# Kernel optimization log

Hardware: AMD Instinct MI355X
Metric: run time of the kernel (lower is better)

The kernel has to match this reference:

```python
import jax, jax.numpy as jnp
import numpy as np

B, T, F = 16, 16384, 32
C = 64          # residual_channels == skip_channels
L = 10          # num_layers
K = 3           # kernel_size
OUT = 1
DILATIONS = [2 ** (i % 10) for i in range(L)]


def causal_conv1d(x, w, b, dilation):
    # x: [B,C_in,T], w: [C_out,C_in,K] -> [B,C_out,T], left-padded (causal)
    pad = (w.shape[-1] - 1) * dilation
    y = jax.lax.conv_general_dilated(
        x, w, window_strides=(1,), padding=[(pad, 0)],
        rhs_dilation=(dilation,), dimension_numbers=('NCT', 'OIT', 'NCT'))
    return y + b[None, :, None]


def conv1x1(x, w, b):
    # x: [B,C_in,T], w: [C_out,C_in] -> [B,C_out,T]
    return jnp.einsum('oi,bit->bot', w, x) + b[None, :, None]


def setup_inputs() -> dict:
    key = jax.random.key(0)
    ks = jax.random.split(key, 16)
    s = 0.1
    inp = {
        'x': jax.random.normal(ks[0], (B, T, F), jnp.float32),
        'w_in': jax.random.normal(ks[1], (C, F, 1), jnp.float32) * s,
        'b_in': jnp.zeros((C,), jnp.float32),
        'fw': jax.random.normal(ks[2], (L, C, C, K), jnp.float32) * s,
        'fb': jnp.zeros((L, C), jnp.float32),
        'gw': jax.random.normal(ks[3], (L, C, C, K), jnp.float32) * s,
        'gb': jnp.zeros((L, C), jnp.float32),
        'rw': jax.random.normal(ks[4], (L, C, C), jnp.float32) * s,
        'rb': jnp.zeros((L, C), jnp.float32),
        'sw': jax.random.normal(ks[5], (L, C, C), jnp.float32) * s,
        'sb': jnp.zeros((L, C), jnp.float32),
        'ow1': jax.random.normal(ks[6], (C, C), jnp.float32) * s,
        'ob1': jnp.zeros((C,), jnp.float32),
        'ow2': jax.random.normal(ks[7], (OUT, C), jnp.float32) * s,
        'ob2': jnp.zeros((OUT,), jnp.float32),
    }
    return inp


def reference(x, w_in, b_in, fw, fb, gw, gb, rw, rb, sw, sb, ow1, ob1, ow2, ob2):
    h = jnp.transpose(x, (0, 2, 1))                 # [B,F,T]
    h = causal_conv1d(h, w_in, b_in, 1)             # [B,C,T] (1x1 causal input conv)
    skip_sum = jnp.zeros_like(h[:, :C, :]) * 0.0
    skip_sum = jnp.zeros((h.shape[0], C, h.shape[2]), h.dtype)
    for i, d in enumerate(DILATIONS):
        filt = jnp.tanh(causal_conv1d(h, fw[i], fb[i], d))
        gate = jax.nn.sigmoid(causal_conv1d(h, gw[i], gb[i], d))
        act = filt * gate
        residual = conv1x1(act, rw[i], rb[i])
        skip = conv1x1(act, sw[i], sb[i])
        h = (h + residual) * 0.7071
        skip_sum = skip_sum + skip
    out = jax.nn.relu(skip_sum)
    out = jax.nn.relu(conv1x1(out, ow1, ob1))
    out = conv1x1(out, ow2, ob2)                    # [B,OUT,T]
    return jnp.transpose(out, (0, 2, 1))            # [B,T,OUT]
```

## Files before the change

kernel.cpp:

```cpp
#include <hip/hip_runtime.h>
#include <math.h>

#define Bn 16
#define Tn 16384
#define Fn 32
#define Cn 64
#define Ln 10
#define ST 76

typedef _Float16 v8h  __attribute__((ext_vector_type(8)));
typedef _Float16 v4h  __attribute__((ext_vector_type(4)));
typedef float    v16f __attribute__((ext_vector_type(16)));
typedef float    v4f  __attribute__((ext_vector_type(4)));

__global__ __launch_bounds__(256) void k_prep(const float* __restrict__ fw,
                                              const float* __restrict__ gw,
                                              const float* __restrict__ rw,
                                              const float* __restrict__ sw,
                                              _Float16* __restrict__ wfgP,
                                              _Float16* __restrict__ rsP)
{
    int gid = blockIdx.x * 256 + threadIdx.x;
    if (gid < Ln * 24576) {
        int l      = gid / 24576;
        int rem    = gid % 24576;
        int chunk  = rem >> 9;
        int within = rem & 511;
        int lane   = within >> 3, j = within & 7;
        int ch32 = chunk & 1;
        int fg   = (chunk >> 1) & 1;
        int kc   = (chunk >> 2) & 3;
        int tap  = chunk >> 4;
        int co = ch32 * 32 + (lane & 31);
        int ci = kc * 16 + (lane >> 5) * 8 + j;
        const float* wsrc = fg ? gw : fw;
        wfgP[gid] = (_Float16)wsrc[((l * 64 + co) * 64 + ci) * 3 + tap];
    }
    int gid2 = gid - Ln * 24576;
    if (gid2 >= 0 && gid2 < Ln * 8192) {
        int l      = gid2 / 8192;
        int rem    = gid2 % 8192;
        int chunk  = rem >> 9;
        int within = rem & 511;
        int lane   = within >> 3, j = within & 7;
        int ch32 = chunk & 1;
        int rsi  = (chunk >> 1) & 1;
        int kc   = chunk >> 2;
        int co = ch32 * 32 + (lane & 31);
        int ci = kc * 16 + (lane >> 5) * 8 + j;
        const float* wsrc = rsi ? sw : rw;
        rsP[gid2] = (_Float16)wsrc[(l * 64 + co) * 64 + ci];
    }
}

__device__ __forceinline__ int xcd_swizzle(int bx, int nblk)
{
    return (bx & 7) * (nblk >> 3) + (bx >> 3);
}

__global__ __launch_bounds__(256) void k_input(const float* __restrict__ x,
                                               const float* __restrict__ w_in,
                                               const float* __restrict__ b_in,
                                               _Float16* __restrict__ h)
{
    __shared__ _Float16 HT[256 * 64];
    const int tid = threadIdx.x;
    const int blk = xcd_swizzle(blockIdx.x, Tn / 256);
    const int t0  = blk * 256;
    const int t   = t0 + tid;
    const int bb  = blockIdx.y;
    const float* xp = x + ((size_t)bb * Tn + t) * Fn;
    float xv[32];
    #pragma unroll
    for (int i = 0; i < 8; ++i) {
        v4f v = *(const v4f*)&xp[i * 4];
        xv[i*4+0] = v[0]; xv[i*4+1] = v[1]; xv[i*4+2] = v[2]; xv[i*4+3] = v[3];
    }
    #pragma unroll
    for (int c8 = 0; c8 < 8; ++c8) {
        v8h o;
        #pragma unroll
        for (int j = 0; j < 8; ++j) {
            int c = c8 * 8 + j;
            float a = b_in[c];
            #pragma unroll
            for (int f = 0; f < 32; ++f) a = fmaf(w_in[c * 32 + f], xv[f], a);
            o[j] = (_Float16)a;
        }
        const int p = (c8 + tid) & 7;
        *(v8h*)&HT[tid * 64 + p * 8] = o;
    }
    __syncthreads();
    _Float16* hp = h + ((size_t)bb * Tn + t0) * 64;
    #pragma unroll
    for (int it = 0; it < 8; ++it) {
        const int g  = it * 256 + tid;
        const int tl = g >> 3, c8 = g & 7;
        const int p  = (c8 + tl) & 7;
        *(v8h*)&hp[g * 8] = *(const v8h*)&HT[tl * 64 + p * 8];
    }
}

__global__ __launch_bounds__(256, 4) void k_layer(
    const _Float16* __restrict__ hin, _Float16* __restrict__ hout,
    _Float16* __restrict__ skip,
    const _Float16* __restrict__ wfg,
    const _Float16* __restrict__ rs,
    const float* __restrict__ fb, const float* __restrict__ gb,
    const float* __restrict__ rb, const float* __restrict__ sb,
    const int dil, const float skip_scale)
{
    __shared__ _Float16 P0[64 * ST];
    __shared__ _Float16 P1[64 * ST];

    const int tid  = threadIdx.x;
    const int lane = tid & 63;
    const int wv   = tid >> 6;
    const int ch32 = wv & 1;
    const int ch   = ch32 * 32;
    const int tw   = (wv >> 1) * 32;
    const int hl   = lane >> 5;
    const int ln31 = lane & 31;
    const int bb   = blockIdx.y;
    const int t0   = xcd_swizzle(blockIdx.x, Tn / 64) * 64;
    const size_t hbase = (size_t)bb * Tn * 64;

    v8h zero8;
    #pragma unroll
    for (int j = 0; j < 8; ++j) zero8[j] = (_Float16)0.f;

    const int s_tl = tid >> 3;
    const int s_c  = (tid & 7) * 8;

#define STAGE(DST, OFF) do {                                                  \
    _Pragma("unroll")                                                         \
    for (int it = 0; it < 2; ++it) {                                          \
        int tl = s_tl + it * 32;                                              \
        int tg = t0 + tl - (OFF);                                             \
        v8h v = zero8;                                                        \
        if (tg >= 0) v = *(const v8h*)&hin[hbase + (size_t)tg * 64 + s_c];    \
        *(v8h*)&(DST)[tl * ST + s_c] = v;                                     \
    } } while (0)

#define WOFF(TAP, KC, FG) (((((TAP) * 4 + (KC)) * 2 + (FG)) * 2 + ch32) * 512 + lane * 8)
#define RSOFF(KC, RSI)    ((((KC) * 2 + (RSI)) * 2 + ch32) * 512 + lane * 8)

#define MFMA_TAP(SRC, TAP) do {                                               \
    _Pragma("unroll")                                                         \
    for (int kc = 0; kc < 4; ++kc) {                                          \
        const int kof = kc * 16 + hl * 8;                                     \
        v8h aF = *(const v8h*)&wfg[WOFF(TAP, kc, 0)];                         \
        v8h aG = *(const v8h*)&wfg[WOFF(TAP, kc, 1)];                         \
        v8h b0 = *(const v8h*)&(SRC)[(tw + ln31) * ST + kof];                 \
        accF = __builtin_amdgcn_mfma_f32_32x32x16_f16(aF, b0, accF, 0, 0, 0); \
        accG = __builtin_amdgcn_mfma_f32_32x32x16_f16(aG, b0, accG, 0, 0, 0); \
    } } while (0)

    v16f accF, accG;
    #pragma unroll
    for (int q = 0; q < 4; ++q) {
        v4f fv = *(const v4f*)&fb[ch + 8 * q + 4 * hl];
        v4f gv = *(const v4f*)&gb[ch + 8 * q + 4 * hl];
        #pragma unroll
        for (int r = 0; r < 4; ++r) {
            accF[q * 4 + r] = fv[r];
            accG[q * 4 + r] = gv[r];
        }
    }

    STAGE(P0, 2 * dil);
    __syncthreads();
    STAGE(P1, dil);
    MFMA_TAP(P0, 0);
    __syncthreads();
    STAGE(P0, 0);
    MFMA_TAP(P1, 1);
    __syncthreads();
    MFMA_TAP(P0, 2);

    #pragma unroll
    for (int q = 0; q < 4; ++q) {
        v4h av;
        #pragma unroll
        for (int r = 0; r < 4; ++r) {
            float f = accF[q * 4 + r];
            float g = accG[q * 4 + r];
            float A = __expf(2.f * f);
            float B = __expf(-g);
            float tA = A + 1.f;
            float den = fmaf(tA, B, tA);
            av[r] = (_Float16)((A - 1.f) * __builtin_amdgcn_rcpf(den));
        }
        *(v4h*)&P1[(tw + ln31) * ST + ch + 8 * q + 4 * hl] = av;
    }
    __syncthreads();

    v16f accR, accS;
    #pragma unroll
    for (int q = 0; q < 4; ++q) {
        v4f rv = *(const v4f*)&rb[ch + 8 * q + 4 * hl];
        v4f sv = *(const v4f*)&sb[ch + 8 * q + 4 * hl];
        #pragma unroll
        for (int r = 0; r < 4; ++r) {
            accR[q * 4 + r] = rv[r];
            accS[q * 4 + r] = sv[r];
        }
    }

    #pragma unroll
    for (int kc = 0; kc < 4; ++kc) {
        const int kof = kc * 16 + hl * 8;
        v8h aR = *(const v8h*)&rs[RSOFF(kc, 0)];
        v8h aS = *(const v8h*)&rs[RSOFF(kc, 1)];
        v8h b0 = *(const v8h*)&P1[(tw + ln31) * ST + kof];
        accR = __builtin_amdgcn_mfma_f32_32x32x16_f16(aR, b0, accR, 0, 0, 0);
        accS = __builtin_amdgcn_mfma_f32_32x32x16_f16(aS, b0, accS, 0, 0, 0);
    }

    #pragma unroll
    for (int q = 0; q < 4; ++q) {
        _Float16* cell = &P0[(tw + ln31) * ST + ch + 8 * q + 4 * hl];
        v4h hv = *(const v4h*)cell;
        v4h hn;
        #pragma unroll
        for (int r = 0; r < 4; ++r)
            hn[r] = (_Float16)(((float)hv[r] + accR[q * 4 + r]) * 0.7071f);
        *(v4h*)cell = hn;
    }
    __syncthreads();

    #pragma unroll
    for (int q = 0; q < 4; ++q) {
        v4h sn;
        #pragma unroll
        for (int r = 0; r < 4; ++r)
            sn[r] = (_Float16)accS[q * 4 + r];
        *(v4h*)&P1[(tw + ln31) * ST + ch + 8 * q + 4 * hl] = sn;
    }
    #pragma unroll
    for (int it = 0; it < 2; ++it) {
        int tl = s_tl + it * 32;
        *(v8h*)&hout[hbase + (size_t)(t0 + tl) * 64 + s_c] = *(const v8h*)&P0[tl * ST + s_c];
    }
    __syncthreads();

    #pragma unroll
    for (int it = 0; it < 2; ++it) {
        int tl = s_tl + it * 32;
        const size_t base = hbase + (size_t)(t0 + tl) * 64 + s_c;
        v8h sk = *(const v8h*)&skip[base];
        v8h pv = *(const v8h*)&P1[tl * ST + s_c];
        v8h sn;
        #pragma unroll
        for (int r = 0; r < 8; ++r)
            sn[r] = (_Float16)((float)sk[r] * skip_scale + (float)pv[r]);
        *(v8h*)&skip[base] = sn;
    }
#undef STAGE
#undef MFMA_TAP
#undef WOFF
#undef RSOFF
}

__global__ __launch_bounds__(256) void k_out(const _Float16* __restrict__ skip,
                                             const float* __restrict__ ow1,
                                             const float* __restrict__ ob1,
                                             const float* __restrict__ ow2,
                                             const float* __restrict__ ob2,
                                             float* __restrict__ out)
{
    const int blk = xcd_swizzle(blockIdx.x, Tn / 256);
    const int t  = blk * 256 + threadIdx.x;
    const int bb = blockIdx.y;
    const _Float16* sp = skip + ((size_t)bb * Tn + t) * 64;
    float y[64];
    #pragma unroll
    for (int i = 0; i < 8; ++i) {
        v8h v = *(const v8h*)&sp[i * 8];
        #pragma unroll
        for (int j = 0; j < 8; ++j) y[i * 8 + j] = fmaxf((float)v[j], 0.f);
    }
    float o = ob2[0];
    for (int co = 0; co < 64; ++co) {
        float a0 = ob1[co], a1 = 0.f;
        #pragma unroll
        for (int ci = 0; ci < 64; ci += 2) {
            a0 = fmaf(ow1[co * 64 + ci],     y[ci],     a0);
            a1 = fmaf(ow1[co * 64 + ci + 1], y[ci + 1], a1);
        }
        o = fmaf(ow2[co], fmaxf(a0 + a1, 0.f), o);
    }
    out[(size_t)bb * Tn + t] = o;
}

extern "C" void kernel_launch(void* const* d_in, const int* in_sizes, int n_in,
                              void* d_out, int out_size, void* d_ws, size_t ws_size,
                              hipStream_t stream)
{
    const float* x    = (const float*)d_in[0];
    const float* w_in = (const float*)d_in[1];
    const float* b_in = (const float*)d_in[2];
    const float* fw   = (const float*)d_in[3];
    const float* fb   = (const float*)d_in[4];
    const float* gw   = (const float*)d_in[5];
    const float* gb   = (const float*)d_in[6];
    const float* rw   = (const float*)d_in[7];
    const float* rb   = (const float*)d_in[8];
    const float* sw   = (const float*)d_in[9];
    const float* sb   = (const float*)d_in[10];
    const float* ow1  = (const float*)d_in[11];
    const float* ob1  = (const float*)d_in[12];
    const float* ow2  = (const float*)d_in[13];
    const float* ob2  = (const float*)d_in[14];
    float* out = (float*)d_out;

    const size_t n = (size_t)Bn * Tn * 64;
    _Float16* hA    = (_Float16*)d_ws;
    _Float16* hB    = hA + n;
    _Float16* skip  = hB + n;
    _Float16* wfg16 = skip + n;
    _Float16* rs16  = wfg16 + (size_t)Ln * 24576;

    dim3 blk(256);
    k_prep<<<dim3((Ln * 24576 + Ln * 8192 + 255) / 256), blk, 0, stream>>>(
        fw, gw, rw, sw, wfg16, rs16);
    k_input<<<dim3(Tn / 256, Bn), blk, 0, stream>>>(x, w_in, b_in, hA);

    const _Float16* cur = hA;
    _Float16* nxt = hB;
    for (int l = 0; l < Ln; ++l) {
        const int d = 1 << l;
        k_layer<<<dim3(Tn / 64, Bn), blk, 0, stream>>>(
            cur, nxt, skip,
            wfg16 + (size_t)l * 24576, rs16 + (size_t)l * 8192,
            fb + l * Cn, gb + l * Cn, rb + l * Cn, sb + l * Cn,
            d, (l == 0) ? 0.f : 1.f);
        const _Float16* tmp = nxt; nxt = (_Float16*)cur; cur = tmp;
    }

    k_out<<<dim3(Tn / 256, Bn), blk, 0, stream>>>(skip, ow1, ob1, ow2, ob2, out);
}
```

Before: 549.6 us.

## Add unified-tile layer kernel for small dilations loading one contiguous halo window

Adds a specialized layer kernel for dilations up to 32 that stages a single contiguous 128-row window (64 halo rows plus 64 output rows) into one shared buffer. All three conv taps then read from that buffer, replacing the original kernel's two separate tiles. The buffer is reused for the activations, the updated residual and the skip values. This is meant to cut redundant global loads and shared memory footprint for the first six layers, at the cost of extra barriers and a second code path.

After: 534.7 us. 2.7% less time.

```diff
diff --git a/kernel.cpp b/kernel.cpp
--- a/kernel.cpp
+++ b/kernel.cpp
@@ -99,6 +99,158 @@
         const int p  = (c8 + tl) & 7;
         *(v8h*)&hp[g * 8] = *(const v8h*)&HT[tl * 64 + p * 8];
     }
+}
+
+__global__ __launch_bounds__(256, 4) void k_layer_u(
+    const _Float16* __restrict__ hin, _Float16* __restrict__ hout,
+    _Float16* __restrict__ skip,
+    const _Float16* __restrict__ wfg,
+    const _Float16* __restrict__ rs,
+    const float* __restrict__ fb, const float* __restrict__ gb,
+    const float* __restrict__ rb, const float* __restrict__ sb,
+    const int dil, const float skip_scale)
+{
+    __shared__ _Float16 UB[128 * ST];
+
+    const int tid  = threadIdx.x;
+    const int lane = tid & 63;
+    const int wv   = tid >> 6;
+    const int ch32 = wv & 1;
+    const int ch   = ch32 * 32;
+    const int tw   = (wv >> 1) * 32;
+    const int hl   = lane >> 5;
+    const int ln31 = lane & 31;
+    const int bb   = blockIdx.y;
+    const int t0   = xcd_swizzle(blockIdx.x, Tn / 64) * 64;
+    const size_t hbase = (size_t)bb * Tn * 64;
+
+    v8h zero8;
+    #pragma unroll
+    for (int j = 0; j < 8; ++j) zero8[j] = (_Float16)0.f;
+
+    const int s_tl = tid >> 3;
+    const int s_c  = (tid & 7) * 8;
+
+#define WOFF(TAP, KC, FG) (((((TAP) * 4 + (KC)) * 2 + (FG)) * 2 + ch32) * 512 + lane * 8)
+#define RSOFF(KC, RSI)    ((((KC) * 2 + (RSI)) * 2 + ch32) * 512 + lane * 8)
+
+    #pragma unroll
+    for (int it = 0; it < 4; ++it) {
+        int row = s_tl + it * 32;
+        int tg  = t0 - 64 + row;
+        v8h v = zero8;
+        if (tg >= 0) v = *(const v8h*)&hin[hbase + (size_t)tg * 64 + s_c];
+        *(v8h*)&UB[row * ST + s_c] = v;
+    }
+
+    v16f accF, accG;
+    #pragma unroll
+    for (int q = 0; q < 4; ++q) {
+        v4f fv = *(const v4f*)&fb[ch + 8 * q + 4 * hl];
+        v4f gv = *(const v4f*)&gb[ch + 8 * q + 4 * hl];
+        #pragma unroll
+        for (int r = 0; r < 4; ++r) {
+            accF[q * 4 + r] = fv[r];
+            accG[q * 4 + r] = gv[r];
+        }
+    }
+    __syncthreads();
+
+    #pragma unroll
+    for (int tap = 0; tap < 3; ++tap) {
+        const int rbase = 64 + tw - (2 - tap) * dil;
+        #pragma unroll
+        for (int kc = 0; kc < 4; ++kc) {
+            const int kof = kc * 16 + hl * 8;
+            v8h aF = *(const v8h*)&wfg[WOFF(tap, kc, 0)];
+            v8h aG = *(const v8h*)&wfg[WOFF(tap, kc, 1)];
+            v8h b0 = *(const v8h*)&UB[(rbase + ln31) * ST + kof];
+            accF = __builtin_amdgcn_mfma_f32_32x32x16_f16(aF, b0, accF, 0, 0, 0);
+            accG = __builtin_amdgcn_mfma_f32_32x32x16_f16(aG, b0, accG, 0, 0, 0);
+        }
+    }
+    __syncthreads();
+
+    #pragma unroll
+    for (int q = 0; q < 4; ++q) {
+        v4h av;
+        #pragma unroll
+        for (int r = 0; r < 4; ++r) {
+            float f = accF[q * 4 + r];
+            float g = accG[q * 4 + r];
+            float A = __expf(2.f * f);
+            float B = __expf(-g);
+            float tA = A + 1.f;
+            float den = fmaf(tA, B, tA);
+            av[r] = (_Float16)((A - 1.f) * __builtin_amdgcn_rcpf(den));
+        }
+        *(v4h*)&UB[(tw + ln31) * ST + ch + 8 * q + 4 * hl] = av;
+    }
+    __syncthreads();
+
+    v16f accR, accS;
+    #pragma unroll
+    for (int q = 0; q < 4; ++q) {
+        v4f rv = *(const v4f*)&rb[ch + 8 * q + 4 * hl];
+        v4f sv = *(const v4f*)&sb[ch + 8 * q + 4 * hl];
+        #pragma unroll
+        for (int r = 0; r < 4; ++r) {
+            accR[q * 4 + r] = rv[r];
+            accS[q * 4 + r] = sv[r];
+        }
+    }
+    #pragma unroll
+    for (int kc = 0; kc < 4; ++kc) {
+        const int kof = kc * 16 + hl * 8;
+        v8h aR = *(const v8h*)&rs[RSOFF(kc, 0)];
+        v8h aS = *(const v8h*)&rs[RSOFF(kc, 1)];
+        v8h b0 = *(const v8h*)&UB[(tw + ln31) * ST + kof];
+        accR = __builtin_amdgcn_mfma_f32_32x32x16_f16(aR, b0, accR, 0, 0, 0);
+        accS = __builtin_amdgcn_mfma_f32_32x32x16_f16(aS, b0, accS, 0, 0, 0);
+    }
+
+    #pragma unroll
+    for (int q = 0; q < 4; ++q) {
+        _Float16* cell = &UB[(64 + tw + ln31) * ST + ch + 8 * q + 4 * hl];
+        v4h hv = *(const v4h*)cell;
+        v4h hn;
+        #pragma unroll
+        for (int r = 0; r < 4; ++r)
+            hn[r] = (_Float16)(((float)hv[r] + accR[q * 4 + r]) * 0.7071f);
+        *(v4h*)cell = hn;
+    }
+    __syncthreads();
+
+    #pragma unroll
+    for (int q = 0; q < 4; ++q) {
+        v4h sn;
+        #pragma unroll
+        for (int r = 0; r < 4; ++r)
+            sn[r] = (_Float16)accS[q * 4 + r];
+        *(v4h*)&UB[(tw + ln31) * ST + ch + 8 * q + 4 * hl] = sn;
+    }
+    __syncthreads();
+
+    #pragma unroll
+    for (int it = 0; it < 2; ++it) {
+        int tl = s_tl + it * 32;
+        *(v8h*)&hout[hbase + (size_t)(t0 + tl) * 64 + s_c] =
+            *(const v8h*)&UB[(64 + tl) * ST + s_c];
+    }
+    #pragma unroll
+    for (int it = 0; it < 2; ++it) {
+        int tl = s_tl + it * 32;
+        const size_t base = hbase + (size_t)(t0 + tl) * 64 + s_c;
+        v8h sk = *(const v8h*)&skip[base];
+        v8h pv = *(const v8h*)&UB[tl * ST + s_c];
+        v8h sn;
+        #pragma unroll
+        for (int r = 0; r < 8; ++r)
+            sn[r] = (_Float16)((float)sk[r] * skip_scale + (float)pv[r]);
+        *(v8h*)&skip[base] = sn;
+    }
+#undef WOFF
+#undef RSOFF
 }
 
 __global__ __launch_bounds__(256, 4) void k_layer(
@@ -330,11 +482,19 @@
     _Float16* nxt = hB;
     for (int l = 0; l < Ln; ++l) {
         const int d = 1 << l;
-        k_layer<<<dim3(Tn / 64, Bn), blk, 0, stream>>>(
-            cur, nxt, skip,
-            wfg16 + (size_t)l * 24576, rs16 + (size_t)l * 8192,
-            fb + l * Cn, gb + l * Cn, rb + l * Cn, sb + l * Cn,
-            d, (l == 0) ? 0.f : 1.f);
+        if (d <= 32) {
+            k_layer_u<<<dim3(Tn / 64, Bn), blk, 0, stream>>>(
+                cur, nxt, skip,
+                wfg16 + (size_t)l * 24576, rs16 + (size_t)l * 8192,
+                fb + l * Cn, gb + l * Cn, rb + l * Cn, sb + l * Cn,
+                d, (l == 0) ? 0.f : 1.f);
+        } else {
+            k_layer<<<dim3(Tn / 64, Bn), blk, 0, stream>>>(
+                cur, nxt, skip,
+                wfg16 + (size_t)l * 24576, rs16 + (size_t)l * 8192,
+                fb + l * Cn, gb + l * Cn, rb + l * Cn, sb + l * Cn,
+                d, 1.f);
+        }
         const _Float16* tmp = nxt; nxt = (_Float16*)cur; cur = tmp;
     }
 
```

## Process two 64-step time tiles per block and skip final layer's h write

Applied to the files above, without the earlier changes.

Each layer block now handles 128 time steps as two 64-step sub-tiles, so every weight fragment loaded from global memory feeds four MFMAs instead of two. The last layer no longer computes or writes the residual h output, since nothing reads it. In exchange, LDS use doubles to four 64x76 half buffers and accumulator register pressure doubles. Both changes can lower occupancy, and the grid has half as many blocks.

New measurement: 635.3 us. +15.6%, slower.

```diff
diff --git a/kernel.cpp b/kernel.cpp
--- a/kernel.cpp
+++ b/kernel.cpp
@@ -101,17 +101,18 @@
     }
 }
 
-__global__ __launch_bounds__(256, 4) void k_layer(
+__global__ __launch_bounds__(256, 4) void k_layer2(
     const _Float16* __restrict__ hin, _Float16* __restrict__ hout,
     _Float16* __restrict__ skip,
-    const _Float16* __restrict__ wfg,
-    const _Float16* __restrict__ rs,
+    const _Float16* __restrict__ wfg, const _Float16* __restrict__ rs,
     const float* __restrict__ fb, const float* __restrict__ gb,
     const float* __restrict__ rb, const float* __restrict__ sb,
-    const int dil, const float skip_scale)
+    const int dil, const float skip_scale, const int write_h)
 {
     __shared__ _Float16 P0[64 * ST];
     __shared__ _Float16 P1[64 * ST];
+    __shared__ _Float16 Q0[64 * ST];
+    __shared__ _Float16 Q1[64 * ST];
 
     const int tid  = threadIdx.x;
     const int lane = tid & 63;
@@ -122,7 +123,8 @@
     const int hl   = lane >> 5;
     const int ln31 = lane & 31;
     const int bb   = blockIdx.y;
-    const int t0   = xcd_swizzle(blockIdx.x, Tn / 64) * 64;
+    const int tA   = xcd_swizzle(blockIdx.x, Tn / 128) * 128;
+    const int tB   = tA + 64;
     const size_t hbase = (size_t)bb * Tn * 64;
 
     v8h zero8;
@@ -132,132 +134,167 @@
     const int s_tl = tid >> 3;
     const int s_c  = (tid & 7) * 8;
 
-#define STAGE(DST, OFF) do {                                                  \
+#define STAGE2(DA, DB, OFF) do {                                              \
     _Pragma("unroll")                                                         \
     for (int it = 0; it < 2; ++it) {                                          \
         int tl = s_tl + it * 32;                                              \
-        int tg = t0 + tl - (OFF);                                             \
-        v8h v = zero8;                                                        \
-        if (tg >= 0) v = *(const v8h*)&hin[hbase + (size_t)tg * 64 + s_c];    \
-        *(v8h*)&(DST)[tl * ST + s_c] = v;                                     \
+        int tgA = tA + tl - (OFF);                                            \
+        v8h vA = zero8;                                                       \
+        if (tgA >= 0) vA = *(const v8h*)&hin[hbase + (size_t)tgA * 64 + s_c]; \
+        *(v8h*)&(DA)[tl * ST + s_c] = vA;                                     \
+        int tgB = tB + tl - (OFF);                                            \
+        v8h vB = zero8;                                                       \
+        if (tgB >= 0) vB = *(const v8h*)&hin[hbase + (size_t)tgB * 64 + s_c]; \
+        *(v8h*)&(DB)[tl * ST + s_c] = vB;                                     \
     } } while (0)
 
 #define WOFF(TAP, KC, FG) (((((TAP) * 4 + (KC)) * 2 + (FG)) * 2 + ch32) * 512 + lane * 8)
 #define RSOFF(KC, RSI)    ((((KC) * 2 + (RSI)) * 2 + ch32) * 512 + lane * 8)
 
-#define MFMA_TAP(SRC, TAP) do {                                               \
+#define MFMA_TAP2(SA, SB, TAP) do {                                           \
     _Pragma("unroll")                                                         \
     for (int kc = 0; kc < 4; ++kc) {                                          \
         const int kof = kc * 16 + hl * 8;                                     \
         v8h aF = *(const v8h*)&wfg[WOFF(TAP, kc, 0)];                         \
         v8h aG = *(const v8h*)&wfg[WOFF(TAP, kc, 1)];                         \
-        v8h b0 = *(const v8h*)&(SRC)[(tw + ln31) * ST + kof];                 \
-        accF = __builtin_amdgcn_mfma_f32_32x32x16_f16(aF, b0, accF, 0, 0, 0); \
-        accG = __builtin_amdgcn_mfma_f32_32x32x16_f16(aG, b0, accG, 0, 0, 0); \
+        v8h bA = *(const v8h*)&(SA)[(tw + ln31) * ST + kof];                  \
+        v8h bB = *(const v8h*)&(SB)[(tw + ln31) * ST + kof];                  \
+        accFA = __builtin_amdgcn_mfma_f32_32x32x16_f16(aF, bA, accFA, 0, 0, 0); \
+        accGA = __builtin_amdgcn_mfma_f32_32x32x16_f16(aG, bA, accGA, 0, 0, 0); \
+        accFB = __builtin_amdgcn_mfma_f32_32x32x16_f16(aF, bB, accFB, 0, 0, 0); \
+        accGB = __builtin_amdgcn_mfma_f32_32x32x16_f16(aG, bB, accGB, 0, 0, 0); \
     } } while (0)
 
-    v16f accF, accG;
+    v16f accFA, accGA, accFB, accGB;
     #pragma unroll
     for (int q = 0; q < 4; ++q) {
         v4f fv = *(const v4f*)&fb[ch + 8 * q + 4 * hl];
         v4f gv = *(const v4f*)&gb[ch + 8 * q + 4 * hl];
         #pragma unroll
         for (int r = 0; r < 4; ++r) {
-            accF[q * 4 + r] = fv[r];
-            accG[q * 4 + r] = gv[r];
-        }
-    }
-
-    STAGE(P0, 2 * dil);
-    __syncthreads();
-    STAGE(P1, dil);
-    MFMA_TAP(P0, 0);
-    __syncthreads();
-    STAGE(P0, 0);
-    MFMA_TAP(P1, 1);
-    __syncthreads();
-    MFMA_TAP(P0, 2);
+            accFA[q*4+r] = fv[r]; accGA[q*4+r] = gv[r];
+            accFB[q*4+r] = fv[r]; accGB[q*4+r] = gv[r];
+        }
+    }
+
+    STAGE2(P0, Q0, 2 * dil);
+    __syncthreads();
+    STAGE2(P1, Q1, dil);
+    MFMA_TAP2(P0, Q0, 0);
+    __syncthreads();
+    STAGE2(P0, Q0, 0);
+    MFMA_TAP2(P1, Q1, 1);
+    __syncthreads();
+    MFMA_TAP2(P0, Q0, 2);
 
     #pragma unroll
     for (int q = 0; q < 4; ++q) {
-        v4h av;
+        v4h avA, avB;
         #pragma unroll
         for (int r = 0; r < 4; ++r) {
-            float f = accF[q * 4 + r];
-            float g = accG[q * 4 + r];
-            float A = __expf(2.f * f);
-            float B = __expf(-g);
-            float tA = A + 1.f;
-            float den = fmaf(tA, B, tA);
-            av[r] = (_Float16)((A - 1.f) * __builtin_amdgcn_rcpf(den));
-        }
-        *(v4h*)&P1[(tw + ln31) * ST + ch + 8 * q + 4 * hl] = av;
-    }
-    __syncthreads();
-
-    v16f accR, accS;
+            {
+                float f = accFA[q * 4 + r], g = accGA[q * 4 + r];
+                float A = __expf(2.f * f), B = __expf(-g);
+                float tAx = A + 1.f;
+                float den = fmaf(tAx, B, tAx);
+                avA[r] = (_Float16)((A - 1.f) * __builtin_amdgcn_rcpf(den));
+            }
+            {
+                float f = accFB[q * 4 + r], g = accGB[q * 4 + r];
+                float A = __expf(2.f * f), B = __expf(-g);
+                float tAx = A + 1.f;
+                float den = fmaf(tAx, B, tAx);
+                avB[r] = (_Float16)((A - 1.f) * __builtin_amdgcn_rcpf(den));
+            }
+        }
+        *(v4h*)&P1[(tw + ln31) * ST + ch + 8 * q + 4 * hl] = avA;
+        *(v4h*)&Q1[(tw + ln31) * ST + ch + 8 * q + 4 * hl] = avB;
+    }
+    __syncthreads();
+
+    v16f accRA, accSA, accRB, accSB;
     #pragma unroll
     for (int q = 0; q < 4; ++q) {
         v4f rv = *(const v4f*)&rb[ch + 8 * q + 4 * hl];
         v4f sv = *(const v4f*)&sb[ch + 8 * q + 4 * hl];
         #pragma unroll
         for (int r = 0; r < 4; ++r) {
-            accR[q * 4 + r] = rv[r];
-            accS[q * 4 + r] = sv[r];
-        }
-    }
-
+            accRA[q*4+r] = rv[r]; accSA[q*4+r] = sv[r];
+            accRB[q*4+r] = rv[r]; accSB[q*4+r] = sv[r];
+        }
+    }
     #pragma unroll
     for (int kc = 0; kc < 4; ++kc) {
         const int kof = kc * 16 + hl * 8;
         v8h aR = *(const v8h*)&rs[RSOFF(kc, 0)];
         v8h aS = *(const v8h*)&rs[RSOFF(kc, 1)];
-        v8h b0 = *(const v8h*)&P1[(tw + ln31) * ST + kof];
-        accR = __builtin_amdgcn_mfma_f32_32x32x16_f16(aR, b0, accR, 0, 0, 0);
-        accS = __builtin_amdgcn_mfma_f32_32x32x16_f16(aS, b0, accS, 0, 0, 0);
-    }
+        v8h bA = *(const v8h*)&P1[(tw + ln31) * ST + kof];
+        v8h bB = *(const v8h*)&Q1[(tw + ln31) * ST + kof];
+        accRA = __builtin_amdgcn_mfma_f32_32x32x16_f16(aR, bA, accRA, 0, 0, 0);
+        accSA = __builtin_amdgcn_mfma_f32_32x32x16_f16(aS, bA, accSA, 0, 0, 0);
+        accRB = __builtin_amdgcn_mfma_f32_32x32x16_f16(aR, bB, accRB, 0, 0, 0);
+        accSB = __builtin_amdgcn_mfma_f32_32x32x16_f16(aS, bB, accSB, 0, 0, 0);
+    }
+
+    if (write_h) {
+        #pragma unroll
+        for (int q = 0; q < 4; ++q) {
+            _Float16* cA = &P0[(tw + ln31) * ST + ch + 8 * q + 4 * hl];
+            _Float16* cB = &Q0[(tw + ln31) * ST + ch + 8 * q + 4 * hl];
+            v4h hA = *(const v4h*)cA, hB = *(const v4h*)cB;
+            v4h nA, nB;
+            #pragma unroll
+            for (int r = 0; r < 4; ++r) {
+                nA[r] = (_Float16)(((float)hA[r] + accRA[q * 4 + r]) * 0.7071f);
+                nB[r] = (_Float16)(((float)hB[r] + accRB[q * 4 + r]) * 0.7071f);
+            }
+            *(v4h*)cA = nA;
+            *(v4h*)cB = nB;
+        }
+    }
+    __syncthreads();
 
     #pragma unroll
     for (int q = 0; q < 4; ++q) {
-        _Float16* cell = &P0[(tw + ln31) * ST + ch + 8 * q + 4 * hl];
-        v4h hv = *(const v4h*)cell;
-        v4h hn;
-        #pragma unroll
-        for (int r = 0; r < 4; ++r)
-            hn[r] = (_Float16)(((float)hv[r] + accR[q * 4 + r]) * 0.7071f);
-        *(v4h*)cell = hn;
-    }
-    __syncthreads();
-
-    #pragma unroll
-    for (int q = 0; q < 4; ++q) {
-        v4h sn;
-        #pragma unroll
-        for (int r = 0; r < 4; ++r)
-            sn[r] = (_Float16)accS[q * 4 + r];
-        *(v4h*)&P1[(tw + ln31) * ST + ch + 8 * q + 4 * hl] = sn;
-    }
+        v4h sA, sB;
+        #pragma unroll
+        for (int r = 0; r < 4; ++r) {
+            sA[r] = (_Float16)accSA[q * 4 + r];
+            sB[r] = (_Float16)accSB[q * 4 + r];
+        }
+        *(v4h*)&P1[(tw + ln31) * ST + ch + 8 * q + 4 * hl] = sA;
+        *(v4h*)&Q1[(tw + ln31) * ST + ch + 8 * q + 4 * hl] = sB;
+    }
+    if (write_h) {
+        #pragma unroll
+        for (int it = 0; it < 2; ++it) {
+            int tl = s_tl + it * 32;
+            *(v8h*)&hout[hbase + (size_t)(tA + tl) * 64 + s_c] = *(const v8h*)&P0[tl * ST + s_c];
+            *(v8h*)&hout[hbase + (size_t)(tB + tl) * 64 + s_c] = *(const v8h*)&Q0[tl * ST + s_c];
+        }
+    }
+    __syncthreads();
+
     #pragma unroll
     for (int it = 0; it < 2; ++it) {
         int tl = s_tl + it * 32;
-        *(v8h*)&hout[hbase + (size_t)(t0 + tl) * 64 + s_c] = *(const v8h*)&P0[tl * ST + s_c];
-    }
-    __syncthreads();
-
-    #pragma unroll
-    for (int it = 0; it < 2; ++it) {
-        int tl = s_tl + it * 32;
-        const size_t base = hbase + (size_t)(t0 + tl) * 64 + s_c;
-        v8h sk = *(const v8h*)&skip[base];
-        v8h pv = *(const v8h*)&P1[tl * ST + s_c];
-        v8h sn;
-        #pragma unroll
-        for (int r = 0; r < 8; ++r)
-            sn[r] = (_Float16)((float)sk[r] * skip_scale + (float)pv[r]);
-        *(v8h*)&skip[base] = sn;
-    }
-#undef STAGE
-#undef MFMA_TAP
+        const size_t baseA = hbase + (size_t)(tA + tl) * 64 + s_c;
+        const size_t baseB = hbase + (size_t)(tB + tl) * 64 + s_c;
+        v8h skA = *(const v8h*)&skip[baseA];
+        v8h skB = *(const v8h*)&skip[baseB];
+        v8h pA = *(const v8h*)&P1[tl * ST + s_c];
+        v8h pB = *(const v8h*)&Q1[tl * ST + s_c];
+        v8h nA, nB;
+        #pragma unroll
+        for (int r = 0; r < 8; ++r) {
+            nA[r] = (_Float16)((float)skA[r] * skip_scale + (float)pA[r]);
+            nB[r] = (_Float16)((float)skB[r] * skip_scale + (float)pB[r]);
+        }
+        *(v8h*)&skip[baseA] = nA;
+        *(v8h*)&skip[baseB] = nB;
+    }
+#undef STAGE2
+#undef MFMA_TAP2
 #undef WOFF
 #undef RSOFF
 }
@@ -330,11 +367,12 @@
     _Float16* nxt = hB;
     for (int l = 0; l < Ln; ++l) {
         const int d = 1 << l;
-        k_layer<<<dim3(Tn / 64, Bn), blk, 0, stream>>>(
+        k_layer2<<<dim3(Tn / 128, Bn), blk, 0, stream>>>(
             cur, nxt, skip,
             wfg16 + (size_t)l * 24576, rs16 + (size_t)l * 8192,
             fb + l * Cn, gb + l * Cn, rb + l * Cn, sb + l * Cn,
-            d, (l == 0) ? 0.f : 1.f);
+            d, (l == 0) ? 0.f : 1.f,
+            (l == Ln - 1) ? 0 : 1);
         const _Float16* tmp = nxt; nxt = (_Float16*)cur; cur = tmp;
     }
 
```
